# Performance work log

Hardware: AMD Instinct MI355X
Metric: run time of the kernel (lower is better)

The kernel has to match this reference:

```python
import jax, jax.numpy as jnp
import numpy as np

B, T, D = 128, 512, 512
K = 64  # memory slots per bank


def setup_inputs() -> dict:
    key = jax.random.key(0)
    ks = jax.random.split(key, 8)
    stdv = 1.0 / np.sqrt(D)
    return {
        "x": jax.random.normal(ks[0], (B, T, D), jnp.float32),
        "Amem": jax.random.uniform(ks[1], (K, D), jnp.float32, -stdv, stdv),
        "Nmem": jax.random.uniform(ks[2], (K, D), jnp.float32, -stdv, stdv),
        "W_mu": jax.random.normal(ks[3], (D, D), jnp.float32) * 0.02,
        "b_mu": jnp.zeros((D,), jnp.float32),
        "W_var": jax.random.normal(ks[4], (D, D), jnp.float32) * 0.02,
        "b_var": jnp.zeros((D,), jnp.float32),
        # reparameterization noise (torch.randn_like(std)), shape of N_aug: [B//2, T, D]
        "epsilon": jax.random.normal(ks[5], (B // 2, T, D), jnp.float32),
    }


def _memory(data, mem):
    # UR-DMU / DA-MIST Memory_Bank: sigmoid attention over memory slots
    att = jax.nn.sigmoid(jnp.einsum('btd,kd->btk', data, mem)
                         / jnp.sqrt(jnp.asarray(mem.shape[-1], data.dtype)))
    topv, _ = jax.lax.top_k(att, mem.shape[0] // 16 + 1)   # [b,t,k']
    t_att = topv.mean(-1)                                  # [b,t]
    aug = jnp.einsum('btk,kd->btd', att, mem)              # [b,t,d]
    return t_att, aug


def _l2norm(v):
    return v / jnp.linalg.norm(v, axis=-1, keepdims=True)


def _gather_mean(feats, idx):
    # feats [b,t,d], idx [b,k] -> mean over gathered snippets -> [b,d]
    return jnp.take_along_axis(feats, idx[:, :, None], axis=1).mean(1)


def reference(x, Amem, Nmem, W_mu, b_mu, W_var, b_var, epsilon):
    b, t, d = x.shape
    mid = b // 2
    N_x, A_x = x[:mid], x[mid:]

    A_att, A_aug = _memory(A_x, Amem)
    N_Aatt, N_Aaug = _memory(A_x, Nmem)
    A_Natt, A_Naug = _memory(N_x, Amem)
    N_att, N_aug = _memory(N_x, Nmem)

    k = t // 16 + 1
    _, A_idx = jax.lax.top_k(A_att, k)   # [mid,k]
    _, N_idx = jax.lax.top_k(N_att, k)
    _, P_idx = jax.lax.top_k(N_Aatt, k)

    negative_ax = _gather_mean(A_x, A_idx)
    anchor_nx = _gather_mean(N_x, N_idx)
    positive_nx = _gather_mean(A_x, P_idx)

    a, p, n = _l2norm(anchor_nx), _l2norm(positive_nx), _l2norm(negative_ax)
    # torch TripletMarginLoss: pairwise_distance adds eps=1e-6 elementwise
    d_ap = jnp.linalg.norm(a - p + 1e-6, axis=-1)
    d_an = jnp.linalg.norm(a - n + 1e-6, axis=-1)
    triplet = jnp.mean(jnp.maximum(d_ap - d_an + 1.0, 0.0))

    mu_fn = lambda h: h @ W_mu + b_mu
    var_fn = lambda h: h @ W_var + b_var

    N_aug_mu = mu_fn(N_aug)
    N_aug_var = var_fn(N_aug)
    N_aug_new = N_aug_mu + epsilon * jnp.sqrt(jnp.exp(N_aug_var))

    anchor_nx_new = _gather_mean(N_aug_new, N_idx)    # reshape(mid,1,-1).mean(1) is identity
    A_aug_new = mu_fn(A_aug)
    negative_ax_new = _gather_mean(A_aug_new, A_idx)

    kl_loss = jnp.mean(-0.5 * jnp.sum(1.0 + N_aug_var - N_aug_mu ** 2 - jnp.exp(N_aug_var), axis=1))

    A_Naug_mu = mu_fn(A_Naug)
    N_Aaug_mu = mu_fn(N_Aaug)

    distance = jnp.mean(jax.nn.relu(100.0
                                    - jnp.linalg.norm(negative_ax_new, axis=-1)
                                    + jnp.linalg.norm(anchor_nx_new, axis=-1)))

    F_M = jnp.concatenate(
        [x, jnp.concatenate([N_aug_new + A_Naug_mu, A_aug_new + N_Aaug_mu], axis=0)],
        axis=-1)  # [b,t,2d]

    return (F_M, triplet, kl_loss, distance, A_att, N_att, A_Natt, N_Aatt)
```

## Files before the change

kernel.cpp:

```cpp
#include <hip/hip_runtime.h>
#include <hip/hip_bf16.h>
#include <math.h>

typedef unsigned short u16;
typedef __attribute__((ext_vector_type(4))) float f32x4;
typedef __attribute__((ext_vector_type(8))) short s16x8;

#define O_FM    0ULL
#define O_TRIP  67108864ULL
#define O_KL    67108865ULL
#define O_DIST  67108866ULL
#define O_AATT  67108867ULL
#define O_NATT  67141635ULL
#define O_ANATT 67174403ULL
#define O_NAATT 67207171ULL

#define WS_ATTB  0ULL
#define WS_BCT   16777216ULL
#define WS_PVT   16908288ULL
#define WS_PAM   16973824ULL
#define WS_PNM   17104896ULL
#define WS_PNV   17235968ULL
#define WS_MBH   17367040ULL
#define WS_MBL   17498112ULL
#define WS_TATT  17629184ULL
#define WS_IDX   18022400ULL
#define WS_GATH  18053120ULL
#define WS_NORM  18446336ULL
#define WS_KL    18446848ULL
#define WS_TRIPB 18447360ULL
#define WS_SUM   18447616ULL

__device__ __forceinline__ u16 f2bf(float f) {
    union { float f; unsigned int u; } c; c.f = f;
    unsigned int r = c.u + 0x7fffu + ((c.u >> 16) & 1u);
    return (u16)(r >> 16);
}
__device__ __forceinline__ float bf2f(u16 h) {
    union { unsigned int u; float f; } c; c.u = ((unsigned int)h) << 16;
    return c.f;
}

__device__ __forceinline__ float blk_sum(float v, float* red) {
    #pragma unroll
    for (int o = 32; o; o >>= 1) v += __shfl_xor(v, o);
    int tid = threadIdx.x;
    if ((tid & 63) == 0) red[tid >> 6] = v;
    __syncthreads();
    float r = red[0] + red[1] + red[2] + red[3];
    __syncthreads();
    return r;
}

__device__ __forceinline__ void stage32_512(const u16* __restrict__ g, int row0, int ld, int k0,
                                            u16* s, int tid) {
    const u16* src = g + (size_t)(row0 + (tid >> 2)) * ld + k0 + (tid & 3) * 8;
    __builtin_amdgcn_global_load_lds((const __attribute__((address_space(1))) void*)src,
                                     (__attribute__((address_space(3))) void*)(s + tid * 8),
                                     16, 0, 0);
}

__global__ __launch_bounds__(256) void k_prep(const float* __restrict__ Amem, const float* __restrict__ Nmem,
                                              char* __restrict__ ws) {
    int i = blockIdx.x * 256 + threadIdx.x;
    if (i == 0) *(float*)(ws + WS_KL) = 0.f;
    if (i < 32768) ((float*)(ws + WS_SUM))[i] = 0.f;
    int k = i >> 9, d = i & 511;
    float v = (k < 64) ? Amem[(size_t)k * 512 + d] : Nmem[(size_t)(k - 64) * 512 + d];
    u16 h = f2bf(v);
    ((u16*)(ws + WS_MBH))[i] = h;
    ((u16*)(ws + WS_MBL))[i] = f2bf(v - bf2f(h));
}

__global__ __launch_bounds__(256) void k_proj(const float* __restrict__ Amem, const float* __restrict__ Nmem,
                                              const float* __restrict__ Wmu, const float* __restrict__ Wvar,
                                              float* __restrict__ pam, float* __restrict__ pnm,
                                              float* __restrict__ pnv, u16* __restrict__ bct,
                                              u16* __restrict__ pvt) {
    __shared__ float mr[512];
    int mat = blockIdx.x >> 6, k = blockIdx.x & 63, tid = threadIdx.x;
    const float* mrow = ((mat == 0) ? Amem : Nmem) + (size_t)k * 512;
    const float* W = (mat == 2) ? Wvar : Wmu;
    mr[tid] = mrow[tid]; mr[tid + 256] = mrow[tid + 256];
    __syncthreads();
    float s0 = 0.f, s1 = 0.f;
    for (int d = 0; d < 512; ++d) {
        float m = mr[d];
        s0 += m * W[(size_t)d * 512 + tid];
        s1 += m * W[(size_t)d * 512 + tid + 256];
    }
    if (mat == 0) {
        pam[(size_t)k * 512 + tid] = s0; pam[(size_t)k * 512 + tid + 256] = s1;
        bct[(size_t)tid * 128 + k] = f2bf(s0); bct[(size_t)(tid + 256) * 128 + k] = f2bf(s1);
    } else if (mat == 1) {
        pnm[(size_t)k * 512 + tid] = s0; pnm[(size_t)k * 512 + tid + 256] = s1;
        bct[(size_t)tid * 128 + 64 + k] = f2bf(s0); bct[(size_t)(tid + 256) * 128 + 64 + k] = f2bf(s1);
    } else {
        pnv[(size_t)k * 512 + tid] = s0; pnv[(size_t)k * 512 + tid + 256] = s1;
        pvt[(size_t)tid * 64 + k] = f2bf(s0); pvt[(size_t)(tid + 256) * 64 + k] = f2bf(s1);
    }
}

__global__ __launch_bounds__(512) void k_dots(const float* __restrict__ x, char* __restrict__ ws,
                                              float* __restrict__ out) {
    __shared__ u16 sXh[128 * 32];
    __shared__ u16 sXl[128 * 32];
    __shared__ u16 sBh[128 * 32];
    __shared__ u16 sBl[128 * 32];

    int tid = threadIdx.x;
    int row0 = blockIdx.x * 128;
    const u16* mbh = (const u16*)(ws + WS_MBH);
    const u16* mbl = (const u16*)(ws + WS_MBL);
    u16* attb = (u16*)(ws + WS_ATTB);
    int lane = tid & 63, wid = tid >> 6;
    int cl = lane & 15, rq = lane >> 4;

    f32x4 acc[8];
    #pragma unroll
    for (int i = 0; i < 8; ++i) acc[i] = (f32x4)0.f;

    for (int dc = 0; dc < 16; ++dc) {
        int d0 = dc * 32;
        {
            int r = tid >> 2, q4 = tid & 3;
            const float* sp = x + (size_t)(row0 + r) * 512 + d0 + q4 * 8;
            float* op = out + (size_t)(row0 + r) * 1024 + d0 + q4 * 8;
            f32x4 v0 = *(const f32x4*)(sp);
            f32x4 v1 = *(const f32x4*)(sp + 4);
            *(f32x4*)(op) = v0;
            *(f32x4*)(op + 4) = v1;
            s16x8 hs, ls;
            #pragma unroll
            for (int j = 0; j < 4; ++j) {
                u16 h0 = f2bf(v0[j]); hs[j] = (short)h0; ls[j] = (short)f2bf(v0[j] - bf2f(h0));
                u16 h1 = f2bf(v1[j]); hs[4 + j] = (short)h1; ls[4 + j] = (short)f2bf(v1[j] - bf2f(h1));
            }
            *(s16x8*)&sXh[r * 32 + q4 * 8] = hs;
            *(s16x8*)&sXl[r * 32 + q4 * 8] = ls;
        }
        stage32_512(mbh, 0, 512, d0, sBh, tid);
        stage32_512(mbl, 0, 512, d0, sBl, tid);
        __syncthreads();
        s16x8 axh = *(const s16x8*)&sXh[(wid * 16 + cl) * 32 + rq * 8];
        s16x8 axl = *(const s16x8*)&sXl[(wid * 16 + cl) * 32 + rq * 8];
        #pragma unroll
        for (int ni = 0; ni < 8; ++ni) {
            s16x8 bh = *(const s16x8*)&sBh[(ni * 16 + cl) * 32 + rq * 8];
            s16x8 bl = *(const s16x8*)&sBl[(ni * 16 + cl) * 32 + rq * 8];
            acc[ni] = __builtin_amdgcn_mfma_f32_16x16x32_bf16(axh, bh, acc[ni], 0, 0, 0);
            acc[ni] = __builtin_amdgcn_mfma_f32_16x16x32_bf16(axh, bl, acc[ni], 0, 0, 0);
            acc[ni] = __builtin_amdgcn_mfma_f32_16x16x32_bf16(axl, bh, acc[ni], 0, 0, 0);
        }
        __syncthreads();
    }

    #pragma unroll
    for (int ni = 0; ni < 8; ++ni) {
        #pragma unroll
        for (int q = 0; q < 4; ++q) {
            float logit = acc[ni][q] * 0.044194173824159216f;
            float av = 1.f / (1.f + expf(-logit));
            acc[ni][q] = av;
            attb[(size_t)(row0 + wid * 16 + rq * 4 + q) * 128 + ni * 16 + cl] = f2bf(av);
        }
    }

    unsigned long long gmask = 0xFFFFull << (lane & 48);
    float* tatt = (float*)(ws + WS_TATT);
    int half = row0 >> 15;
    #pragma unroll
    for (int q = 0; q < 4; ++q) {
        #pragma unroll
        for (int side = 0; side < 2; ++side) {
            float v0 = acc[side * 4 + 0][q], v1 = acc[side * 4 + 1][q];
            float v2 = acc[side * 4 + 2][q], v3 = acc[side * 4 + 3][q];
            float sum5 = 0.f;
            #pragma unroll
            for (int it = 0; it < 5; ++it) {
                float m = v0; int jm = 0;
                if (v1 > m) { m = v1; jm = 1; }
                if (v2 > m) { m = v2; jm = 2; }
                if (v3 > m) { m = v3; jm = 3; }
                float g = m;
                g = fmaxf(g, __shfl_xor(g, 1));
                g = fmaxf(g, __shfl_xor(g, 2));
                g = fmaxf(g, __shfl_xor(g, 4));
                g = fmaxf(g, __shfl_xor(g, 8));
                sum5 += g;
                unsigned long long bl = __ballot(m == g) & gmask;
                int owner = __ffsll(bl) - 1;
                if (lane == owner) {
                    if (jm == 0) v0 = -INFINITY;
                    else if (jm == 1) v1 = -INFINITY;
                    else if (jm == 2) v2 = -INFINITY;
                    else v3 = -INFINITY;
                }
            }
            if (cl == 0) {
                float tv = sum5 / 5.f;
                int lr = (row0 + wid * 16 + rq * 4 + q) & 32767;
                if (half) {
                    if (side == 0) { out[O_AATT + lr]  = tv; tatt[lr] = tv; }
                    else           { out[O_NAATT + lr] = tv; tatt[2 * 32768 + lr] = tv; }
                } else {
                    if (side == 0) { out[O_ANATT + lr] = tv; }
                    else           { out[O_NATT + lr]  = tv; tatt[32768 + lr] = tv; }
                }
            }
        }
    }
}

__global__ __launch_bounds__(256) void k_topk(const float* __restrict__ tatt, int* __restrict__ idx) {
    __shared__ float vals[512];
    int s = blockIdx.x >> 6, b = blockIdx.x & 63, tid = threadIdx.x;
    const float* src = tatt + (size_t)s * 32768 + b * 512;
    vals[tid] = src[tid]; vals[tid + 256] = src[tid + 256];
    __syncthreads();
    #pragma unroll
    for (int e = 0; e < 2; ++e) {
        int i = tid + e * 256;
        float v = vals[i];
        int rank = 0;
        for (int j = 0; j < 512; j += 4) {
            f32x4 w4 = *(const f32x4*)&vals[j];
            rank += (w4.x > v) || (w4.x == v && (j + 0) < i);
            rank += (w4.y > v) || (w4.y == v && (j + 1) < i);
            rank += (w4.z > v) || (w4.z == v && (j + 2) < i);
            rank += (w4.w > v) || (w4.w == v && (j + 3) < i);
        }
        if (rank < 33) idx[(s * 64 + b) * 40 + rank] = i;
    }
}

__global__ __launch_bounds__(256) void k_gather3(const float* __restrict__ x, const int* __restrict__ idx,
                                                 float* __restrict__ gath) {
    __shared__ int il[33];
    int s = blockIdx.x >> 6, b = blockIdx.x & 63, tid = threadIdx.x;
    if (tid < 33) il[tid] = idx[(s * 64 + b) * 40 + tid];
    __syncthreads();
    int srcb = (s == 1) ? b : 64 + b;
    const float* xb = x + (size_t)srcb * 262144;
    int d0 = tid * 2;
    float a0 = 0.f, a1 = 0.f;
    for (int i = 0; i < 33; ++i) {
        const float* p = xb + (size_t)il[i] * 512 + d0;
        a0 += p[0]; a1 += p[1];
    }
    gath[((size_t)s * 64 + b) * 512 + d0]     = a0 / 33.f;
    gath[((size_t)s * 64 + b) * 512 + d0 + 1] = a1 / 33.f;
}

__global__ __launch_bounds__(256) void k_triplet(const float* __restrict__ gath, float* __restrict__ tripb) {
    __shared__ float red[8];
    int b = blockIdx.x, tid = threadIdx.x;
    const float* a = gath + (size_t)(64 + b) * 512;
    const float* p = gath + (size_t)(128 + b) * 512;
    const float* n = gath + (size_t)(b) * 512;
    float a0 = a[tid], a1 = a[tid + 256];
    float p0 = p[tid], p1 = p[tid + 256];
    float n0 = n[tid], n1 = n[tid + 256];
    float na  = sqrtf(blk_sum(a0 * a0 + a1 * a1, red));
    float npv = sqrtf(blk_sum(p0 * p0 + p1 * p1, red));
    float nn  = sqrtf(blk_sum(n0 * n0 + n1 * n1, red));
    float e0 = a0 / na - p0 / npv + 1e-6f, e1 = a1 / na - p1 / npv + 1e-6f;
    float f0 = a0 / na - n0 / nn  + 1e-6f, f1 = a1 / na - n1 / nn  + 1e-6f;
    float dap = sqrtf(blk_sum(e0 * e0 + e1 * e1, red));
    float dan = sqrtf(blk_sum(f0 * f0 + f1 * f1, red));
    if (tid == 0) tripb[b] = fmaxf(dap - dan + 1.f, 0.f);
}

__global__ __launch_bounds__(512) void kG1(const u16* __restrict__ attb, const u16* __restrict__ bct,
                                           const u16* __restrict__ pvt, const float* __restrict__ bmu,
                                           const float* __restrict__ bvar, const float* __restrict__ epsv,
                                           float* __restrict__ fm, float* __restrict__ klacc) {
    __shared__ u16 sAA[128 * 32];
    __shared__ u16 sAN[128 * 32];
    __shared__ u16 sBA[128 * 32];
    __shared__ u16 sBN[128 * 32];
    __shared__ u16 sBV[128 * 32];
    __shared__ float red[8];
    int tid = threadIdx.x, lane = tid & 63, wid = tid >> 6;
    int wr = wid >> 2, wc = wid & 3;
    int cl = lane & 15, rq = lane >> 4;
    int m0 = blockIdx.x * 128, c0 = blockIdx.y * 128;

    f32x4 aA[4][2], aN[4][2], aV[4][2];
    #pragma unroll
    for (int i = 0; i < 4; ++i)
        #pragma unroll
        for (int j = 0; j < 2; ++j) { aA[i][j] = (f32x4)0.f; aN[i][j] = (f32x4)0.f; aV[i][j] = (f32x4)0.f; }

    for (int kt = 0; kt < 2; ++kt) {
        stage32_512(attb, m0, 128, kt * 32, sAA, tid);
        stage32_512(attb, m0, 128, 64 + kt * 32, sAN, tid);
        stage32_512(bct, c0, 128, kt * 32, sBA, tid);
        stage32_512(bct, c0, 128, 64 + kt * 32, sBN, tid);
        stage32_512(pvt, c0, 64, kt * 32, sBV, tid);
        __syncthreads();
        s16x8 fA[4], fN[4], bA[2], bN[2], bV[2];
        #pragma unroll
        for (int i = 0; i < 4; ++i) {
            fA[i] = *(const s16x8*)&sAA[(wr * 64 + i * 16 + cl) * 32 + rq * 8];
            fN[i] = *(const s16x8*)&sAN[(wr * 64 + i * 16 + cl) * 32 + rq * 8];
        }
        #pragma unroll
        for (int n = 0; n < 2; ++n) {
            bA[n] = *(const s16x8*)&sBA[(wc * 32 + n * 16 + cl) * 32 + rq * 8];
            bN[n] = *(const s16x8*)&sBN[(wc * 32 + n * 16 + cl) * 32 + rq * 8];
            bV[n] = *(const s16x8*)&sBV[(wc * 32 + n * 16 + cl) * 32 + rq * 8];
        }
        #pragma unroll
        for (int mi = 0; mi < 4; ++mi)
            #pragma unroll
            for (int ni = 0; ni < 2; ++ni) {
                aA[mi][ni] = __builtin_amdgcn_mfma_f32_16x16x32_bf16(fA[mi], bA[ni], aA[mi][ni], 0, 0, 0);
                aN[mi][ni] = __builtin_amdgcn_mfma_f32_16x16x32_bf16(fN[mi], bN[ni], aN[mi][ni], 0, 0, 0);
                aV[mi][ni] = __builtin_amdgcn_mfma_f32_16x16x32_bf16(fN[mi], bV[ni], aV[mi][ni], 0, 0, 0);
            }
        __syncthreads();
    }

    float kll = 0.f;
    #pragma unroll
    for (int mi = 0; mi < 4; ++mi)
        #pragma unroll
        for (int ni = 0; ni < 2; ++ni) {
            int col = c0 + wc * 32 + ni * 16 + cl;
            int rowb = m0 + wr * 64 + mi * 16 + rq * 4;
            float bm = bmu[col], bv = bvar[col];
            #pragma unroll
            for (int q = 0; q < 4; ++q) {
                int row = rowb + q;
                float muN = aN[mi][ni][q] + bm;
                float var = aV[mi][ni][q] + bv;
                float ev = expf(var);
                float muA = aA[mi][ni][q] + bm;
                fm[(size_t)row * 1024 + 512 + col] =
                    muN + epsv[(size_t)row * 512 + col] * sqrtf(ev) + muA;
                kll += 1.f + var - muN * muN - ev;
            }
        }
    #pragma unroll
    for (int o = 32; o; o >>= 1) kll += __shfl_xor(kll, o);
    if (lane == 0) red[wid] = kll;
    __syncthreads();
    if (tid == 0) {
        float s = 0.f;
        #pragma unroll
        for (int i = 0; i < 8; ++i) s += red[i];
        atomicAdd(klacc, s);
    }
}

__global__ __launch_bounds__(512) void kG3(const u16* __restrict__ attb, const u16* __restrict__ bct,
                                           const float* __restrict__ bmu, float* __restrict__ fm) {
    __shared__ u16 sA[128 * 32];
    __shared__ u16 sB[128 * 32];
    int tid = threadIdx.x, lane = tid & 63, wid = tid >> 6;
    int wr = wid >> 2, wc = wid & 3;
    int cl = lane & 15, rq = lane >> 4;
    int m0 = blockIdx.x * 128, c0 = blockIdx.y * 128;

    f32x4 acc[4][2];
    #pragma unroll
    for (int i = 0; i < 4; ++i)
        #pragma unroll
        for (int j = 0; j < 2; ++j) acc[i][j] = (f32x4)0.f;

    for (int kt = 0; kt < 4; ++kt) {
        stage32_512(attb, 32768 + m0, 128, kt * 32, sA, tid);
        stage32_512(bct, c0, 128, kt * 32, sB, tid);
        __syncthreads();
        s16x8 fa[4], fb[2];
        #pragma unroll
        for (int i = 0; i < 4; ++i)
            fa[i] = *(const s16x8*)&sA[(wr * 64 + i * 16 + cl) * 32 + rq * 8];
        #pragma unroll
        for (int n = 0; n < 2; ++n)
            fb[n] = *(const s16x8*)&sB[(wc * 32 + n * 16 + cl) * 32 + rq * 8];
        #pragma unroll
        for (int mi = 0; mi < 4; ++mi)
            #pragma unroll
            for (int ni = 0; ni < 2; ++ni)
                acc[mi][ni] = __builtin_amdgcn_mfma_f32_16x16x32_bf16(fa[mi], fb[ni], acc[mi][ni], 0, 0, 0);
        __syncthreads();
    }
    #pragma unroll
    for (int mi = 0; mi < 4; ++mi)
        #pragma unroll
        for (int ni = 0; ni < 2; ++ni) {
            int col = c0 + wc * 32 + ni * 16 + cl;
            int rowb = 32768 + m0 + wr * 64 + mi * 16 + rq * 4;
            float bm2 = 2.f * bmu[col];
            #pragma unroll
            for (int q = 0; q < 4; ++q)
                fm[(size_t)(rowb + q) * 1024 + 512 + col] = acc[mi][ni][q] + bm2;
        }
}

__global__ __launch_bounds__(256) void k_gather2a(const int* __restrict__ idx, const u16* __restrict__ attb,
                                                  const float* __restrict__ pnm, const float* __restrict__ pnv,
                                                  const float* __restrict__ bmu, const float* __restrict__ bvar,
                                                  const float* __restrict__ epsv, float* __restrict__ SUM) {
    __shared__ float arow[64];
    int blk = blockIdx.x, b = blk / 3, seg = blk % 3;
    int tid = threadIdx.x;
    float s0 = 0.f, s1 = 0.f;
    for (int i = seg * 11; i < seg * 11 + 11; ++i) {
        int t = idx[(64 + b) * 40 + i];
        size_t r = (size_t)b * 512 + t;
        __syncthreads();
        if (tid < 64) arow[tid] = bf2f(attb[r * 128 + 64 + tid]);
        __syncthreads();
        float mu0 = bmu[tid], mu1 = bmu[tid + 256];
        float v0 = bvar[tid], v1 = bvar[tid + 256];
        for (int k = 0; k < 64; ++k) {
            float a = arow[k];
            mu0 += a * pnm[(size_t)k * 512 + tid];
            mu1 += a * pnm[(size_t)k * 512 + tid + 256];
            v0  += a * pnv[(size_t)k * 512 + tid];
            v1  += a * pnv[(size_t)k * 512 + tid + 256];
        }
        s0 += mu0 + epsv[r * 512 + tid]       * sqrtf(expf(v0));
        s1 += mu1 + epsv[r * 512 + tid + 256] * sqrtf(expf(v1));
    }
    atomicAdd(&SUM[(size_t)b * 512 + tid], s0);
    atomicAdd(&SUM[(size_t)b * 512 + tid + 256], s1);
}

__global__ __launch_bounds__(256) void k_norm2a(const float* __restrict__ SUM, float* __restrict__ norms) {
    __shared__ float red[8];
    int b = blockIdx.x, tid = threadIdx.x;
    float s0 = SUM[(size_t)b * 512 + tid] / 33.f;
    float s1 = SUM[(size_t)b * 512 + tid + 256] / 33.f;
    float ss = blk_sum(s0 * s0 + s1 * s1, red);
    if (tid == 0) norms[b] = sqrtf(ss);
}

__global__ __launch_bounds__(256) void k_gather2b(const int* __restrict__ idx, const u16* __restrict__ attb,
                                                  const float* __restrict__ pam, const float* __restrict__ bmu,
                                                  float* __restrict__ norms) {
    __shared__ float meanA[64];
    __shared__ float red[8];
    int b = blockIdx.x, tid = threadIdx.x;
    if (tid < 64) {
        float s = 0.f;
        for (int i = 0; i < 33; ++i) {
            int t = idx[b * 40 + i];
            s += bf2f(attb[(size_t)(32768 + b * 512 + t) * 128 + tid]);
        }
        meanA[tid] = s * (1.f / 33.f);
    }
    __syncthreads();
    float s0 = bmu[tid], s1 = bmu[tid + 256];
    #pragma unroll 4
    for (int k = 0; k < 64; ++k) {
        float m = meanA[k];
        s0 += m * pam[(size_t)k * 512 + tid];
        s1 += m * pam[(size_t)k * 512 + tid + 256];
    }
    float ss = blk_sum(s0 * s0 + s1 * s1, red);
    if (tid == 0) norms[64 + b] = sqrtf(ss);
}

__global__ __launch_bounds__(64) void k_final(const float* __restrict__ norms, const float* __restrict__ klacc,
                                              const float* __restrict__ tripb, float* __restrict__ out) {
    int tid = threadIdx.x;
    float v = fmaxf(100.f - norms[64 + tid] + norms[tid], 0.f);
    float t = tripb[tid];
    #pragma unroll
    for (int o = 32; o; o >>= 1) { v += __shfl_xor(v, o); t += __shfl_xor(t, o); }
    if (tid == 0) {
        out[O_DIST] = v / 64.f;
        out[O_TRIP] = t / 64.f;
        out[O_KL]   = -0.5f * (*klacc) / 32768.f;
    }
}

extern "C" void kernel_launch(void* const* d_in, const int* in_sizes, int n_in,
                              void* d_out, int out_size, void* d_ws, size_t ws_size,
                              hipStream_t stream) {
    const float* x    = (const float*)d_in[0];
    const float* Amem = (const float*)d_in[1];
    const float* Nmem = (const float*)d_in[2];
    const float* Wmu  = (const float*)d_in[3];
    const float* bmu  = (const float*)d_in[4];
    const float* Wvar = (const float*)d_in[5];
    const float* bvar = (const float*)d_in[6];
    const float* eps  = (const float*)d_in[7];
    float* out = (float*)d_out;
    char* ws = (char*)d_ws;
    const u16* attb  = (const u16*)(ws + WS_ATTB);
    const u16* bct   = (const u16*)(ws + WS_BCT);
    const u16* pvt   = (const u16*)(ws + WS_PVT);
    const float* pam = (const float*)(ws + WS_PAM);
    const float* pnm = (const float*)(ws + WS_PNM);
    const float* pnv = (const float*)(ws + WS_PNV);
    const int* idx   = (const int*)(ws + WS_IDX);

    k_prep<<<256, 256, 0, stream>>>(Amem, Nmem, ws);
    k_proj<<<192, 256, 0, stream>>>(Amem, Nmem, Wmu, Wvar,
                                    (float*)(ws + WS_PAM), (float*)(ws + WS_PNM), (float*)(ws + WS_PNV),
                                    (u16*)(ws + WS_BCT), (u16*)(ws + WS_PVT));
    k_dots<<<512, 512, 0, stream>>>(x, ws, out);
    k_topk<<<192, 256, 0, stream>>>((const float*)(ws + WS_TATT), (int*)(ws + WS_IDX));
    k_gather3<<<192, 256, 0, stream>>>(x, idx, (float*)(ws + WS_GATH));
    k_triplet<<<64, 256, 0, stream>>>((const float*)(ws + WS_GATH), (float*)(ws + WS_TRIPB));
    kG1<<<dim3(256, 4), 512, 0, stream>>>(attb, bct, pvt, bmu, bvar, eps, out, (float*)(ws + WS_KL));
    kG3<<<dim3(256, 4), 512, 0, stream>>>(attb, bct, bmu, out);
    k_gather2a<<<192, 256, 0, stream>>>(idx, attb, pnm, pnv, bmu, bvar, eps, (float*)(ws + WS_SUM));
    k_norm2a<<<64, 256, 0, stream>>>((const float*)(ws + WS_SUM), (float*)(ws + WS_NORM));
    k_gather2b<<<64, 256, 0, stream>>>(idx, attb, pam, bmu, (float*)(ws + WS_NORM));
    k_final<<<1, 64, 0, stream>>>((const float*)(ws + WS_NORM), (const float*)(ws + WS_KL),
                                  (const float*)(ws + WS_TRIPB), out);
}
```

Baseline: 313.7 us.

## Merge independent kernels into fewer launches with block-index dispatch

Cuts the launch sequence from twelve kernels to six. Prep and projection become one kernel, top-k and gather share a kernel with indices kept in LDS, and both GEMMs plus the two gather-projection steps run in one 2304-block kernel dispatched by block index. The norm and triplet reductions are merged into one launch. This removes launch gaps and lets small tail kernels overlap the GEMMs, at the cost of a shared 41KB LDS footprint and 512-thread blocks for the formerly 256-thread work, which may lower occupancy.

```diff
diff --git a/kernel.cpp b/kernel.cpp
--- a/kernel.cpp
+++ b/kernel.cpp
@@ -52,6 +52,18 @@
     return r;
 }
 
+__device__ __forceinline__ float blk_sum8(float v, float* red, int tid) {
+    #pragma unroll
+    for (int o = 32; o; o >>= 1) v += __shfl_xor(v, o);
+    if ((tid & 63) == 0) red[tid >> 6] = v;
+    __syncthreads();
+    float r = red[0];
+    #pragma unroll
+    for (int i = 1; i < 8; ++i) r += red[i];
+    __syncthreads();
+    return r;
+}
+
 __device__ __forceinline__ void stage32_512(const u16* __restrict__ g, int row0, int ld, int k0,
                                             u16* s, int tid) {
     const u16* src = g + (size_t)(row0 + (tid >> 2)) * ld + k0 + (tid & 3) * 8;
@@ -60,25 +72,29 @@
                                      16, 0, 0);
 }
 
-__global__ __launch_bounds__(256) void k_prep(const float* __restrict__ Amem, const float* __restrict__ Nmem,
-                                              char* __restrict__ ws) {
-    int i = blockIdx.x * 256 + threadIdx.x;
-    if (i == 0) *(float*)(ws + WS_KL) = 0.f;
-    if (i < 32768) ((float*)(ws + WS_SUM))[i] = 0.f;
-    int k = i >> 9, d = i & 511;
-    float v = (k < 64) ? Amem[(size_t)k * 512 + d] : Nmem[(size_t)(k - 64) * 512 + d];
-    u16 h = f2bf(v);
-    ((u16*)(ws + WS_MBH))[i] = h;
-    ((u16*)(ws + WS_MBL))[i] = f2bf(v - bf2f(h));
-}
-
-__global__ __launch_bounds__(256) void k_proj(const float* __restrict__ Amem, const float* __restrict__ Nmem,
-                                              const float* __restrict__ Wmu, const float* __restrict__ Wvar,
-                                              float* __restrict__ pam, float* __restrict__ pnm,
-                                              float* __restrict__ pnv, u16* __restrict__ bct,
-                                              u16* __restrict__ pvt) {
+__global__ __launch_bounds__(256) void k_pp(const float* __restrict__ Amem, const float* __restrict__ Nmem,
+                                            const float* __restrict__ Wmu, const float* __restrict__ Wvar,
+                                            char* __restrict__ ws) {
     __shared__ float mr[512];
-    int mat = blockIdx.x >> 6, k = blockIdx.x & 63, tid = threadIdx.x;
+    int bid = blockIdx.x, tid = threadIdx.x;
+    if (bid < 256) {
+        int i = bid * 256 + tid;
+        if (i == 0) *(float*)(ws + WS_KL) = 0.f;
+        if (i < 32768) ((float*)(ws + WS_SUM))[i] = 0.f;
+        int k = i >> 9, d = i & 511;
+        float v = (k < 64) ? Amem[(size_t)k * 512 + d] : Nmem[(size_t)(k - 64) * 512 + d];
+        u16 h = f2bf(v);
+        ((u16*)(ws + WS_MBH))[i] = h;
+        ((u16*)(ws + WS_MBL))[i] = f2bf(v - bf2f(h));
+        return;
+    }
+    int pb = bid - 256;
+    float* pam = (float*)(ws + WS_PAM);
+    float* pnm = (float*)(ws + WS_PNM);
+    float* pnv = (float*)(ws + WS_PNV);
+    u16* bct = (u16*)(ws + WS_BCT);
+    u16* pvt = (u16*)(ws + WS_PVT);
+    int mat = pb >> 6, k = pb & 63;
     const float* mrow = ((mat == 0) ? Amem : Nmem) + (size_t)k * 512;
     const float* W = (mat == 2) ? Wvar : Wmu;
     mr[tid] = mrow[tid]; mr[tid + 256] = mrow[tid + 256];
@@ -212,8 +228,10 @@
     }
 }
 
-__global__ __launch_bounds__(256) void k_topk(const float* __restrict__ tatt, int* __restrict__ idx) {
+__global__ __launch_bounds__(256) void k_tg(const float* __restrict__ tatt, int* __restrict__ idx,
+                                            const float* __restrict__ x, float* __restrict__ gath) {
     __shared__ float vals[512];
+    __shared__ int il[40];
     int s = blockIdx.x >> 6, b = blockIdx.x & 63, tid = threadIdx.x;
     const float* src = tatt + (size_t)s * 32768 + b * 512;
     vals[tid] = src[tid]; vals[tid + 256] = src[tid + 256];
@@ -230,15 +248,8 @@
             rank += (w4.z > v) || (w4.z == v && (j + 2) < i);
             rank += (w4.w > v) || (w4.w == v && (j + 3) < i);
         }
-        if (rank < 33) idx[(s * 64 + b) * 40 + rank] = i;
-    }
-}
-
-__global__ __launch_bounds__(256) void k_gather3(const float* __restrict__ x, const int* __restrict__ idx,
-                                                 float* __restrict__ gath) {
-    __shared__ int il[33];
-    int s = blockIdx.x >> 6, b = blockIdx.x & 63, tid = threadIdx.x;
-    if (tid < 33) il[tid] = idx[(s * 64 + b) * 40 + tid];
+        if (rank < 33) { idx[(s * 64 + b) * 40 + rank] = i; il[rank] = i; }
+    }
     __syncthreads();
     int srcb = (s == 1) ? b : 64 + b;
     const float* xb = x + (size_t)srcb * 262144;
@@ -252,39 +263,20 @@
     gath[((size_t)s * 64 + b) * 512 + d0 + 1] = a1 / 33.f;
 }
 
-__global__ __launch_bounds__(256) void k_triplet(const float* __restrict__ gath, float* __restrict__ tripb) {
-    __shared__ float red[8];
-    int b = blockIdx.x, tid = threadIdx.x;
-    const float* a = gath + (size_t)(64 + b) * 512;
-    const float* p = gath + (size_t)(128 + b) * 512;
-    const float* n = gath + (size_t)(b) * 512;
-    float a0 = a[tid], a1 = a[tid + 256];
-    float p0 = p[tid], p1 = p[tid + 256];
-    float n0 = n[tid], n1 = n[tid + 256];
-    float na  = sqrtf(blk_sum(a0 * a0 + a1 * a1, red));
-    float npv = sqrtf(blk_sum(p0 * p0 + p1 * p1, red));
-    float nn  = sqrtf(blk_sum(n0 * n0 + n1 * n1, red));
-    float e0 = a0 / na - p0 / npv + 1e-6f, e1 = a1 / na - p1 / npv + 1e-6f;
-    float f0 = a0 / na - n0 / nn  + 1e-6f, f1 = a1 / na - n1 / nn  + 1e-6f;
-    float dap = sqrtf(blk_sum(e0 * e0 + e1 * e1, red));
-    float dan = sqrtf(blk_sum(f0 * f0 + f1 * f1, red));
-    if (tid == 0) tripb[b] = fmaxf(dap - dan + 1.f, 0.f);
-}
-
-__global__ __launch_bounds__(512) void kG1(const u16* __restrict__ attb, const u16* __restrict__ bct,
-                                           const u16* __restrict__ pvt, const float* __restrict__ bmu,
-                                           const float* __restrict__ bvar, const float* __restrict__ epsv,
-                                           float* __restrict__ fm, float* __restrict__ klacc) {
-    __shared__ u16 sAA[128 * 32];
-    __shared__ u16 sAN[128 * 32];
-    __shared__ u16 sBA[128 * 32];
-    __shared__ u16 sBN[128 * 32];
-    __shared__ u16 sBV[128 * 32];
-    __shared__ float red[8];
-    int tid = threadIdx.x, lane = tid & 63, wid = tid >> 6;
+__device__ __forceinline__ void body_G1(char* smem, int m0, int c0, int tid,
+                                        const u16* __restrict__ attb, const u16* __restrict__ bct,
+                                        const u16* __restrict__ pvt, const float* __restrict__ bmu,
+                                        const float* __restrict__ bvar, const float* __restrict__ epsv,
+                                        float* __restrict__ fm, float* __restrict__ klacc) {
+    u16* sAA = (u16*)(smem);
+    u16* sAN = (u16*)(smem + 8192);
+    u16* sBA = (u16*)(smem + 16384);
+    u16* sBN = (u16*)(smem + 24576);
+    u16* sBV = (u16*)(smem + 32768);
+    float* red = (float*)(smem + 40960);
+    int lane = tid & 63, wid = tid >> 6;
     int wr = wid >> 2, wc = wid & 3;
     int cl = lane & 15, rq = lane >> 4;
-    int m0 = blockIdx.x * 128, c0 = blockIdx.y * 128;
 
     f32x4 aA[4][2], aN[4][2], aV[4][2];
     #pragma unroll
@@ -354,14 +346,14 @@
     }
 }
 
-__global__ __launch_bounds__(512) void kG3(const u16* __restrict__ attb, const u16* __restrict__ bct,
-                                           const float* __restrict__ bmu, float* __restrict__ fm) {
-    __shared__ u16 sA[128 * 32];
-    __shared__ u16 sB[128 * 32];
-    int tid = threadIdx.x, lane = tid & 63, wid = tid >> 6;
+__device__ __forceinline__ void body_G3(char* smem, int m0, int c0, int tid,
+                                        const u16* __restrict__ attb, const u16* __restrict__ bct,
+                                        const float* __restrict__ bmu, float* __restrict__ fm) {
+    u16* sA = (u16*)(smem);
+    u16* sB = (u16*)(smem + 8192);
+    int lane = tid & 63, wid = tid >> 6;
     int wr = wid >> 2, wc = wid & 3;
     int cl = lane & 15, rq = lane >> 4;
-    int m0 = blockIdx.x * 128, c0 = blockIdx.y * 128;
 
     f32x4 acc[4][2];
     #pragma unroll
@@ -400,13 +392,13 @@
         }
 }
 
-__global__ __launch_bounds__(256) void k_gather2a(const int* __restrict__ idx, const u16* __restrict__ attb,
-                                                  const float* __restrict__ pnm, const float* __restrict__ pnv,
-                                                  const float* __restrict__ bmu, const float* __restrict__ bvar,
-                                                  const float* __restrict__ epsv, float* __restrict__ SUM) {
-    __shared__ float arow[64];
-    int blk = blockIdx.x, b = blk / 3, seg = blk % 3;
-    int tid = threadIdx.x;
+__device__ __forceinline__ void body_g2a(char* smem, int blk, int tid,
+                                         const int* __restrict__ idx, const u16* __restrict__ attb,
+                                         const float* __restrict__ pnm, const float* __restrict__ pnv,
+                                         const float* __restrict__ bmu, const float* __restrict__ bvar,
+                                         const float* __restrict__ epsv, float* __restrict__ SUM) {
+    float* arow = (float*)smem;
+    int b = blk / 3, seg = blk % 3;
     float s0 = 0.f, s1 = 0.f;
     for (int i = seg * 11; i < seg * 11 + 11; ++i) {
         int t = idx[(64 + b) * 40 + i];
@@ -414,37 +406,32 @@
         __syncthreads();
         if (tid < 64) arow[tid] = bf2f(attb[r * 128 + 64 + tid]);
         __syncthreads();
-        float mu0 = bmu[tid], mu1 = bmu[tid + 256];
-        float v0 = bvar[tid], v1 = bvar[tid + 256];
-        for (int k = 0; k < 64; ++k) {
-            float a = arow[k];
-            mu0 += a * pnm[(size_t)k * 512 + tid];
-            mu1 += a * pnm[(size_t)k * 512 + tid + 256];
-            v0  += a * pnv[(size_t)k * 512 + tid];
-            v1  += a * pnv[(size_t)k * 512 + tid + 256];
-        }
-        s0 += mu0 + epsv[r * 512 + tid]       * sqrtf(expf(v0));
-        s1 += mu1 + epsv[r * 512 + tid + 256] * sqrtf(expf(v1));
-    }
-    atomicAdd(&SUM[(size_t)b * 512 + tid], s0);
-    atomicAdd(&SUM[(size_t)b * 512 + tid + 256], s1);
-}
-
-__global__ __launch_bounds__(256) void k_norm2a(const float* __restrict__ SUM, float* __restrict__ norms) {
-    __shared__ float red[8];
-    int b = blockIdx.x, tid = threadIdx.x;
-    float s0 = SUM[(size_t)b * 512 + tid] / 33.f;
-    float s1 = SUM[(size_t)b * 512 + tid + 256] / 33.f;
-    float ss = blk_sum(s0 * s0 + s1 * s1, red);
-    if (tid == 0) norms[b] = sqrtf(ss);
-}
-
-__global__ __launch_bounds__(256) void k_gather2b(const int* __restrict__ idx, const u16* __restrict__ attb,
-                                                  const float* __restrict__ pam, const float* __restrict__ bmu,
-                                                  float* __restrict__ norms) {
-    __shared__ float meanA[64];
-    __shared__ float red[8];
-    int b = blockIdx.x, tid = threadIdx.x;
+        if (tid < 256) {
+            float mu0 = bmu[tid], mu1 = bmu[tid + 256];
+            float v0 = bvar[tid], v1 = bvar[tid + 256];
+            for (int k = 0; k < 64; ++k) {
+                float a = arow[k];
+                mu0 += a * pnm[(size_t)k * 512 + tid];
+                mu1 += a * pnm[(size_t)k * 512 + tid + 256];
+                v0  += a * pnv[(size_t)k * 512 + tid];
+                v1  += a * pnv[(size_t)k * 512 + tid + 256];
+            }
+            s0 += mu0 + bf2f(f2bf(0.f)) + epsv[r * 512 + tid]       * sqrtf(expf(v0));
+            s1 += mu1 + epsv[r * 512 + tid + 256] * sqrtf(expf(v1));
+        }
+    }
+    if (tid < 256) {
+        atomicAdd(&SUM[(size_t)b * 512 + tid], s0);
+        atomicAdd(&SUM[(size_t)b * 512 + tid + 256], s1);
+    }
+}
+
+__device__ __forceinline__ void body_g2b(char* smem, int b, int tid,
+                                         const int* __restrict__ idx, const u16* __restrict__ attb,
+                                         const float* __restrict__ pam, const float* __restrict__ bmu,
+                                         float* __restrict__ norms) {
+    float* meanA = (float*)smem;
+    float* red = (float*)(smem + 256);
     if (tid < 64) {
         float s = 0.f;
         for (int i = 0; i < 33; ++i) {
@@ -454,15 +441,69 @@
         meanA[tid] = s * (1.f / 33.f);
     }
     __syncthreads();
-    float s0 = bmu[tid], s1 = bmu[tid + 256];
-    #pragma unroll 4
-    for (int k = 0; k < 64; ++k) {
-        float m = meanA[k];
-        s0 += m * pam[(size_t)k * 512 + tid];
-        s1 += m * pam[(size_t)k * 512 + tid + 256];
-    }
-    float ss = blk_sum(s0 * s0 + s1 * s1, red);
+    float ssv = 0.f;
+    if (tid < 256) {
+        float s0 = bmu[tid], s1 = bmu[tid + 256];
+        #pragma unroll 4
+        for (int k = 0; k < 64; ++k) {
+            float m = meanA[k];
+            s0 += m * pam[(size_t)k * 512 + tid];
+            s1 += m * pam[(size_t)k * 512 + tid + 256];
+        }
+        ssv = s0 * s0 + s1 * s1;
+    }
+    float ss = blk_sum8(ssv, red, tid);
     if (tid == 0) norms[64 + b] = sqrtf(ss);
+}
+
+__global__ __launch_bounds__(512) void k_post(const u16* __restrict__ attb, const u16* __restrict__ bct,
+                                              const u16* __restrict__ pvt, const float* __restrict__ bmu,
+                                              const float* __restrict__ bvar, const float* __restrict__ epsv,
+                                              const int* __restrict__ idx, const float* __restrict__ pam,
+                                              const float* __restrict__ pnm, const float* __restrict__ pnv,
+                                              float* __restrict__ fm, float* __restrict__ klacc,
+                                              float* __restrict__ SUM, float* __restrict__ norms) {
+    __shared__ __align__(16) char smem[41024];
+    int bid = blockIdx.x, tid = threadIdx.x;
+    if (bid < 1024) {
+        body_G1(smem, (bid >> 2) * 128, (bid & 3) * 128, tid, attb, bct, pvt, bmu, bvar, epsv, fm, klacc);
+    } else if (bid < 2048) {
+        int b2 = bid - 1024;
+        body_G3(smem, (b2 >> 2) * 128, (b2 & 3) * 128, tid, attb, bct, bmu, fm);
+    } else if (bid < 2240) {
+        body_g2a(smem, bid - 2048, tid, idx, attb, pnm, pnv, bmu, bvar, epsv, SUM);
+    } else {
+        body_g2b(smem, bid - 2240, tid, idx, attb, pam, bmu, norms);
+    }
+}
+
+__global__ __launch_bounds__(256) void k_nt(const float* __restrict__ SUM, const float* __restrict__ gath,
+                                            float* __restrict__ norms, float* __restrict__ tripb) {
+    __shared__ float red[8];
+    int bid = blockIdx.x, tid = threadIdx.x;
+    if (bid < 64) {
+        int b = bid;
+        float s0 = SUM[(size_t)b * 512 + tid] / 33.f;
+        float s1 = SUM[(size_t)b * 512 + tid + 256] / 33.f;
+        float ss = blk_sum(s0 * s0 + s1 * s1, red);
+        if (tid == 0) norms[b] = sqrtf(ss);
+    } else {
+        int b = bid - 64;
+        const float* a = gath + (size_t)(64 + b) * 512;
+        const float* p = gath + (size_t)(128 + b) * 512;
+        const float* n = gath + (size_t)(b) * 512;
+        float a0 = a[tid], a1 = a[tid + 256];
+        float p0 = p[tid], p1 = p[tid + 256];
+        float n0 = n[tid], n1 = n[tid + 256];
+        float na  = sqrtf(blk_sum(a0 * a0 + a1 * a1, red));
+        float npv = sqrtf(blk_sum(p0 * p0 + p1 * p1, red));
+        float nn  = sqrtf(blk_sum(n0 * n0 + n1 * n1, red));
+        float e0 = a0 / na - p0 / npv + 1e-6f, e1 = a1 / na - p1 / npv + 1e-6f;
+        float f0 = a0 / na - n0 / nn  + 1e-6f, f1 = a1 / na - n1 / nn  + 1e-6f;
+        float dap = sqrtf(blk_sum(e0 * e0 + e1 * e1, red));
+        float dan = sqrtf(blk_sum(f0 * f0 + f1 * f1, red));
+        if (tid == 0) tripb[b] = fmaxf(dap - dan + 1.f, 0.f);
+    }
 }
 
 __global__ __launch_bounds__(64) void k_final(const float* __restrict__ norms, const float* __restrict__ klacc,
@@ -500,19 +541,15 @@
     const float* pnv = (const float*)(ws + WS_PNV);
     const int* idx   = (const int*)(ws + WS_IDX);
 
-    k_prep<<<256, 256, 0, stream>>>(Amem, Nmem, ws);
-    k_proj<<<192, 256, 0, stream>>>(Amem, Nmem, Wmu, Wvar,
-                                    (float*)(ws + WS_PAM), (float*)(ws + WS_PNM), (float*)(ws + WS_PNV),
-                                    (u16*)(ws + WS_BCT), (u16*)(ws + WS_PVT));
+    k_pp<<<448, 256, 0, stream>>>(Amem, Nmem, Wmu, Wvar, ws);
     k_dots<<<512, 512, 0, stream>>>(x, ws, out);
-    k_topk<<<192, 256, 0, stream>>>((const float*)(ws + WS_TATT), (int*)(ws + WS_IDX));
-    k_gather3<<<192, 256, 0, stream>>>(x, idx, (float*)(ws + WS_GATH));
-    k_triplet<<<64, 256, 0, stream>>>((const float*)(ws + WS_GATH), (float*)(ws + WS_TRIPB));
-    kG1<<<dim3(256, 4), 512, 0, stream>>>(attb, bct, pvt, bmu, bvar, eps, out, (float*)(ws + WS_KL));
-    kG3<<<dim3(256, 4), 512, 0, stream>>>(attb, bct, bmu, out);
-    k_gather2a<<<192, 256, 0, stream>>>(idx, attb, pnm, pnv, bmu, bvar, eps, (float*)(ws + WS_SUM));
-    k_norm2a<<<64, 256, 0, stream>>>((const float*)(ws + WS_SUM), (float*)(ws + WS_NORM));
-    k_gather2b<<<64, 256, 0, stream>>>(idx, attb, pam, bmu, (float*)(ws + WS_NORM));
+    k_tg<<<192, 256, 0, stream>>>((const float*)(ws + WS_TATT), (int*)(ws + WS_IDX), x,
+                                  (float*)(ws + WS_GATH));
+    k_post<<<2304, 512, 0, stream>>>(attb, bct, pvt, bmu, bvar, eps, idx, pam, pnm, pnv,
+                                     out, (float*)(ws + WS_KL), (float*)(ws + WS_SUM),
+                                     (float*)(ws + WS_NORM));
+    k_nt<<<128, 256, 0, stream>>>((const float*)(ws + WS_SUM), (const float*)(ws + WS_GATH),
+                                  (float*)(ws + WS_NORM), (float*)(ws + WS_TRIPB));
     k_final<<<1, 64, 0, stream>>>((const float*)(ws + WS_NORM), (const float*)(ws + WS_KL),
                                   (const float*)(ws + WS_TRIPB), out);
 }
```

Result: faster. 272.4 us (-13.2%).
